# Performance work log

Measured on AMD Instinct MI355X. Metric: run time of the kernel, lower is better.

## Reference

```python
import jax, jax.numpy as jnp
import numpy as np

N_FEATURES = 256
SEQ_LEN = 128
N_HIDDEN = 30
N_LAYERS = 2
BATCH = 1024


def _lstm_layer(x, w_ih, w_hh, b_ih, b_hh):
    # x: [B, T, I]; w_ih: [4H, I]; w_hh: [4H, H]; biases: [4H]
    # PyTorch gate order: i, f, g, o
    B = x.shape[0]
    H = w_hh.shape[1]
    # precompute input contribution for all timesteps: [B, T, 4H]
    xg = jnp.einsum('bti,gi->btg', x, w_ih) + (b_ih + b_hh)
    xg = jnp.swapaxes(xg, 0, 1)  # [T, B, 4H]

    def step(carry, xg_t):
        h, c = carry
        gates = xg_t + h @ w_hh.T  # [B, 4H]
        i, f, g, o = jnp.split(gates, 4, axis=-1)
        i = jax.nn.sigmoid(i)
        f = jax.nn.sigmoid(f)
        g = jnp.tanh(g)
        o = jax.nn.sigmoid(o)
        c = f * c + i * g
        h = o * jnp.tanh(c)
        return (h, c), h

    h0 = jnp.zeros((B, H), dtype=x.dtype)
    c0 = jnp.zeros((B, H), dtype=x.dtype)
    _, hs = jax.lax.scan(step, (h0, c0), xg)
    return jnp.swapaxes(hs, 0, 1)  # [B, T, H]


def setup_inputs() -> dict:
    key = jax.random.key(0)
    ks = jax.random.split(key, 12)
    s_in = 1.0 / np.sqrt(N_HIDDEN)
    G = 4 * N_HIDDEN
    inp = {
        'x': jax.random.normal(ks[0], (BATCH, SEQ_LEN, N_FEATURES), dtype=jnp.float32),
        'w_ih0': jax.random.uniform(ks[1], (G, N_FEATURES), jnp.float32, -s_in, s_in),
        'w_hh0': jax.random.uniform(ks[2], (G, N_HIDDEN), jnp.float32, -s_in, s_in),
        'b_ih0': jax.random.uniform(ks[3], (G,), jnp.float32, -s_in, s_in),
        'b_hh0': jax.random.uniform(ks[4], (G,), jnp.float32, -s_in, s_in),
        'w_ih1': jax.random.uniform(ks[5], (G, N_HIDDEN), jnp.float32, -s_in, s_in),
        'w_hh1': jax.random.uniform(ks[6], (G, N_HIDDEN), jnp.float32, -s_in, s_in),
        'b_ih1': jax.random.uniform(ks[7], (G,), jnp.float32, -s_in, s_in),
        'b_hh1': jax.random.uniform(ks[8], (G,), jnp.float32, -s_in, s_in),
        'w_lin': jax.random.uniform(ks[9], (1, N_HIDDEN * SEQ_LEN), jnp.float32, -s_in, s_in),
        'b_lin': jax.random.uniform(ks[10], (1,), jnp.float32, -s_in, s_in),
    }
    return inp


def reference(x, w_ih0, w_hh0, b_ih0, b_hh0, w_ih1, w_hh1, b_ih1, b_hh1, w_lin, b_lin):
    h1 = _lstm_layer(x, w_ih0, w_hh0, b_ih0, b_hh0)   # [B, T, H]
    h2 = _lstm_layer(h1, w_ih1, w_hh1, b_ih1, b_hh1)  # [B, T, H]
    flat = h2.reshape(h2.shape[0], -1)                 # [B, T*H]
    return flat @ w_lin.T + b_lin                      # [B, 1]
```

## Files before the change

### kernel.cpp

```cpp
#include <hip/hip_runtime.h>

#define T_SEQ 128
#define NF 256
#define NH 30
#define NG 120
#define NBATCH 1024
#define M_ROWS (NBATCH * T_SEQ)

#define BIAS_OFF 0
#define BHI_OFF  1024
#define BLO_OFF  (BHI_OFF + 65536)
#define XG_OFF_B (BLO_OFF + 65536)

typedef __attribute__((ext_vector_type(8))) short short8;
typedef __attribute__((ext_vector_type(4))) float float4v;
typedef __attribute__((ext_vector_type(2))) float v2f;

__device__ __forceinline__ short bf16_of(float f) {
  union { float f; unsigned u; } v; v.f = f;
  unsigned r = v.u + 0x7fffu + ((v.u >> 16) & 1u);
  return (short)(r >> 16);
}
__device__ __forceinline__ float f_of_bf16(short s) {
  union { unsigned u; float f; } v; v.u = ((unsigned)(unsigned short)s) << 16;
  return v.f;
}

__device__ __forceinline__ float rl(float v, int j) {
  return __int_as_float(__builtin_amdgcn_readlane(__float_as_int(v), j));
}
__device__ __forceinline__ float fast_rcp(float x) { return __builtin_amdgcn_rcpf(x); }
__device__ __forceinline__ float act_mix(float x, float kIn, float kOut, float cOut) {
  float e = __expf(-kIn * x);
  float r = fast_rcp(1.0f + e);
  return fmaf(kOut, r, cOut);
}
__device__ __forceinline__ float tanh_fast(float x) {
  float e = __expf(-2.0f * x);
  float r = fast_rcp(1.0f + e);
  return fmaf(2.0f, r, -1.0f);
}
__device__ __forceinline__ v2f fma2(float s, v2f b, v2f c) {
  v2f a = {s, s};
  return __builtin_elementwise_fma(a, b, c);
}

__global__ void prep_kernel(const float* __restrict__ w_ih0,
                            const float* __restrict__ b_ih0,
                            const float* __restrict__ b_hh0,
                            unsigned char* __restrict__ ws) {
  int gid = blockIdx.x * 256 + threadIdx.x;
  float* bias = (float*)(ws + BIAS_OFF);
  if (gid < 128) bias[gid] = (gid < NG) ? (b_ih0[gid] + b_hh0[gid]) : 0.0f;

  int lane = gid & 63;
  int ts = gid >> 6;
  int t = ts >> 3, s = ts & 7;
  int n = s * 16 + (lane & 15);
  int k0 = t * 32 + (lane >> 4) * 8;

  short8 hi, lo;
#pragma unroll
  for (int j = 0; j < 8; ++j) {
    float v = (n < NG) ? w_ih0[n * NF + k0 + j] : 0.0f;
    short h = bf16_of(v);
    hi[j] = h;
    lo[j] = bf16_of(v - f_of_bf16(h));
  }
  *(short8*)(ws + BHI_OFF + (size_t)gid * 16) = hi;
  *(short8*)(ws + BLO_OFF + (size_t)gid * 16) = lo;
}

__global__ __launch_bounds__(256, 3) void gemm_xg(const float* __restrict__ x,
                                                  const unsigned char* __restrict__ ws,
                                                  float* __restrict__ xg) {
  __shared__ short lds_B[2][8 * 2 * 64 * 8];
  const int tid = threadIdx.x;
  const int lane = tid & 63;
  const int wave = tid >> 6;
  const int r15 = lane & 15;
  const int quad = lane >> 4;
  const int rowbase = blockIdx.x * 128 + wave * 32;

  const short* __restrict__ Bhi = (const short*)(ws + BHI_OFF);
  const short* __restrict__ Blo = (const short*)(ws + BLO_OFF);
  const float* __restrict__ bias = (const float*)(ws + BIAS_OFF);

  float4v acc[2][8];
#pragma unroll
  for (int s = 0; s < 8; ++s) {
    float b = bias[s * 16 + r15];
    float4v bv = {b, b, b, b};
    acc[0][s] = bv;
    acc[1][s] = bv;
  }

  const float* xptr[2];
  xptr[0] = x + (size_t)(rowbase + r15) * NF + quad * 8;
  xptr[1] = x + (size_t)(rowbase + 16 + r15) * NF + quad * 8;

#pragma unroll
  for (int i = 0; i < 2; ++i) {
    int s = wave * 2 + i;
    const short* ghi = Bhi + ((size_t)(0 * 8 + s) * 64 + lane) * 8;
    const short* glo = Blo + ((size_t)(0 * 8 + s) * 64 + lane) * 8;
    short* lhi = &lds_B[0][(s * 2 + 0) * 64 * 8];
    short* llo = &lds_B[0][(s * 2 + 1) * 64 * 8];
    __builtin_amdgcn_global_load_lds((const __attribute__((address_space(1))) void*)ghi,
                                     (__attribute__((address_space(3))) void*)lhi, 16, 0, 0);
    __builtin_amdgcn_global_load_lds((const __attribute__((address_space(1))) void*)glo,
                                     (__attribute__((address_space(3))) void*)llo, 16, 0, 0);
  }

  short8 ahi[2], alo[2];
#pragma unroll
  for (int g = 0; g < 2; ++g) {
    float4 p0 = *(const float4*)(xptr[g] + 0);
    float4 p1 = *(const float4*)(xptr[g] + 4);
    float f[8] = {p0.x, p0.y, p0.z, p0.w, p1.x, p1.y, p1.z, p1.w};
#pragma unroll
    for (int j = 0; j < 8; ++j) {
      short h = bf16_of(f[j]);
      ahi[g][j] = h;
      alo[g][j] = bf16_of(f[j] - f_of_bf16(h));
    }
  }
  __syncthreads();

  for (int t = 0; t < 8; ++t) {
    const int buf = t & 1;
    float4 anx[2][2];
    if (t < 7) {
#pragma unroll
      for (int i = 0; i < 2; ++i) {
        int s = wave * 2 + i;
        const short* ghi = Bhi + ((size_t)((t + 1) * 8 + s) * 64 + lane) * 8;
        const short* glo = Blo + ((size_t)((t + 1) * 8 + s) * 64 + lane) * 8;
        short* lhi = &lds_B[buf ^ 1][(s * 2 + 0) * 64 * 8];
        short* llo = &lds_B[buf ^ 1][(s * 2 + 1) * 64 * 8];
        __builtin_amdgcn_global_load_lds((const __attribute__((address_space(1))) void*)ghi,
                                         (__attribute__((address_space(3))) void*)lhi, 16, 0, 0);
        __builtin_amdgcn_global_load_lds((const __attribute__((address_space(1))) void*)glo,
                                         (__attribute__((address_space(3))) void*)llo, 16, 0, 0);
      }
#pragma unroll
      for (int g = 0; g < 2; ++g) {
        anx[g][0] = *(const float4*)(xptr[g] + (t + 1) * 32);
        anx[g][1] = *(const float4*)(xptr[g] + (t + 1) * 32 + 4);
      }
    }

#pragma unroll
    for (int s = 0; s < 8; ++s) {
      const short8 bh = *(const short8*)&lds_B[buf][((s * 2 + 0) * 64 + lane) * 8];
      const short8 bl = *(const short8*)&lds_B[buf][((s * 2 + 1) * 64 + lane) * 8];
#pragma unroll
      for (int g = 0; g < 2; ++g) {
        acc[g][s] = __builtin_amdgcn_mfma_f32_16x16x32_bf16(ahi[g], bh, acc[g][s], 0, 0, 0);
        acc[g][s] = __builtin_amdgcn_mfma_f32_16x16x32_bf16(ahi[g], bl, acc[g][s], 0, 0, 0);
        acc[g][s] = __builtin_amdgcn_mfma_f32_16x16x32_bf16(alo[g], bh, acc[g][s], 0, 0, 0);
      }
    }

    if (t < 7) {
#pragma unroll
      for (int g = 0; g < 2; ++g) {
        float f[8] = {anx[g][0].x, anx[g][0].y, anx[g][0].z, anx[g][0].w,
                      anx[g][1].x, anx[g][1].y, anx[g][1].z, anx[g][1].w};
#pragma unroll
        for (int j = 0; j < 8; ++j) {
          short h = bf16_of(f[j]);
          ahi[g][j] = h;
          alo[g][j] = bf16_of(f[j] - f_of_bf16(h));
        }
      }
    }
    __syncthreads();
  }

#pragma unroll
  for (int g = 0; g < 2; ++g) {
    const int row0 = rowbase + g * 16 + quad * 4;
#pragma unroll
    for (int s = 0; s < 8; ++s) {
      const int col = s * 16 + r15;
      if (col < NG) {
#pragma unroll
        for (int i = 0; i < 4; ++i) {
          xg[(size_t)(row0 + i) * NG + col] = acc[g][s][i];
        }
      }
    }
  }
}

__global__ __launch_bounds__(64, 1) void lstm_fused(const float* __restrict__ xg,
                                                    const float* __restrict__ w_hh0,
                                                    const float* __restrict__ w_ih1,
                                                    const float* __restrict__ w_hh1,
                                                    const float* __restrict__ b_ih1,
                                                    const float* __restrict__ b_hh1,
                                                    const float* __restrict__ w_lin,
                                                    const float* __restrict__ b_lin,
                                                    float* __restrict__ out) {
  const int b = blockIdx.x;
  const int lane = threadIdx.x;
  const bool hiHalf = lane >= 32;
  const int l = hiHalf ? (lane - 32) : lane;
  const int lc = (l < NH) ? l : (NH - 1);
  const int gA = hiHalf ? (60 + lc) : lc;
  const int gB = gA + NH;

  const float kInA = hiHalf ? 2.0f : 1.0f;
  const float kOutA = hiHalf ? 2.0f : 1.0f;
  const float cOutA = hiHalf ? -1.0f : 0.0f;

  v2f wAB0[NH], vAB1[NH], uAB1[NH];
#pragma unroll
  for (int j = 0; j < NH; ++j) {
    wAB0[j] = (v2f){w_hh0[gA * NH + j], w_hh0[gB * NH + j]};
    vAB1[j] = (v2f){w_ih1[gA * NH + j], w_ih1[gB * NH + j]};
    uAB1[j] = (v2f){w_hh1[gA * NH + j], w_hh1[gB * NH + j]};
  }
#pragma unroll
  for (int j = 0; j < NH; ++j) {
    asm volatile("" : "+v"(wAB0[j]), "+v"(vAB1[j]), "+v"(uAB1[j]));
  }
  const float bA1 = b_ih1[gA] + b_hh1[gA];
  const float bB1 = b_ih1[gB] + b_hh1[gB];

  const float* __restrict__ xgb = xg + (size_t)b * T_SEQ * NG;

  float a0A = act_mix(xgb[gA], kInA, kOutA, cOutA);
  float a0B = act_mix(xgb[gB], 1.0f, 1.0f, 0.0f);
  float gg0 = __shfl_down(a0A, 32);
  float oo0 = __shfl_down(a0B, 32);
  float c0 = a0A * gg0;
  float h0 = oo0 * tanh_fast(c0);
  float h1 = 0.0f, c1 = 0.0f, acc = 0.0f;
  float wl_cur = w_lin[lc];

#pragma unroll 1
  for (int t = 0; t < T_SEQ; ++t) {
    const int tn = (t + 1 < T_SEQ) ? (t + 1) : (T_SEQ - 1);
    float xnA = xgb[tn * NG + gA];
    float xnB = xgb[tn * NG + gB];
    float wl_nxt = w_lin[tn * NH + lc];

    v2f s1v = {bA1, bB1}, s1v2 = {0.0f, 0.0f};
    v2f s1u = {0.0f, 0.0f}, s1u2 = {0.0f, 0.0f};
    v2f s0n = {0.0f, 0.0f}, s0n2 = {0.0f, 0.0f};
#pragma unroll
    for (int j = 0; j < NH; j += 2) {
      float xj = rl(h0, j);
      float xj1 = rl(h0, j + 1);
      float hj = rl(h1, j);
      float hj1 = rl(h1, j + 1);
      s1v = fma2(xj, vAB1[j], s1v);
      s1u = fma2(hj, uAB1[j], s1u);
      s0n = fma2(xj, wAB0[j], s0n);
      s1v2 = fma2(xj1, vAB1[j + 1], s1v2);
      s1u2 = fma2(hj1, uAB1[j + 1], s1u2);
      s0n2 = fma2(xj1, wAB0[j + 1], s0n2);
    }
    v2f s1 = (s1v + s1v2) + (s1u + s1u2);
    v2f s0 = (s0n + s0n2) + (v2f){xnA, xnB};

    float a1A = act_mix(s1.x, kInA, kOutA, cOutA);
    float a1B = act_mix(s1.y, 1.0f, 1.0f, 0.0f);
    float gg1 = __shfl_down(a1A, 32);
    float oo1 = __shfl_down(a1B, 32);
    c1 = fmaf(a1B, c1, a1A * gg1);
    h1 = oo1 * tanh_fast(c1);
    acc = fmaf(h1, wl_cur, acc);

    a0A = act_mix(s0.x, kInA, kOutA, cOutA);
    a0B = act_mix(s0.y, 1.0f, 1.0f, 0.0f);
    gg0 = __shfl_down(a0A, 32);
    oo0 = __shfl_down(a0B, 32);
    c0 = fmaf(a0B, c0, a0A * gg0);
    h0 = oo0 * tanh_fast(c0);

    wl_cur = wl_nxt;
  }

  if (lane >= NH) acc = 0.0f;
#pragma unroll
  for (int off = 32; off > 0; off >>= 1) acc += __shfl_xor(acc, off);
  if (lane == 0) out[b] = acc + b_lin[0];
}

extern "C" void kernel_launch(void* const* d_in, const int* in_sizes, int n_in,
                              void* d_out, int out_size, void* d_ws, size_t ws_size,
                              hipStream_t stream) {
  (void)in_sizes; (void)n_in; (void)out_size; (void)ws_size;
  const float* x     = (const float*)d_in[0];
  const float* w_ih0 = (const float*)d_in[1];
  const float* w_hh0 = (const float*)d_in[2];
  const float* b_ih0 = (const float*)d_in[3];
  const float* b_hh0 = (const float*)d_in[4];
  const float* w_ih1 = (const float*)d_in[5];
  const float* w_hh1 = (const float*)d_in[6];
  const float* b_ih1 = (const float*)d_in[7];
  const float* b_hh1 = (const float*)d_in[8];
  const float* w_lin = (const float*)d_in[9];
  const float* b_lin = (const float*)d_in[10];
  unsigned char* ws = (unsigned char*)d_ws;
  float* out = (float*)d_out;
  float* xg = (float*)(ws + XG_OFF_B);

  prep_kernel<<<16, 256, 0, stream>>>(w_ih0, b_ih0, b_hh0, ws);
  gemm_xg<<<M_ROWS / 128, 256, 0, stream>>>(x, ws, xg);
  lstm_fused<<<NBATCH, 64, 0, stream>>>(xg, w_hh0, w_ih1, w_hh1,
                                        b_ih1, b_hh1, w_lin, b_lin, out);
}
```

Measured before the change: 312.0 us.

## Split fused LSTM into per-layer recurrences with MFMA GEMM for layer-1 input projection

Replaces the single fused two-layer recurrence kernel with a layer-0 recurrence kernel, a bf16 hi/lo split MFMA GEMM computing the layer-1 input projection for all timesteps, and a layer-1 recurrence kernel. Layer-0 hidden states are written in place into the xg buffer as packed bf16 hi/lo pairs. This cuts the per-step serial work in each recurrence from three 30-wide dot products to one, shortening the critical dependency chain. In exchange it adds two kernel launches, an extra round trip of the xg buffer through memory, and some precision loss from the split-bf16 layer-1 projection.

```diff
diff --git a/kernel.cpp b/kernel.cpp
--- a/kernel.cpp
+++ b/kernel.cpp
@@ -7,10 +7,13 @@
 #define NBATCH 1024
 #define M_ROWS (NBATCH * T_SEQ)
 
-#define BIAS_OFF 0
-#define BHI_OFF  1024
-#define BLO_OFF  (BHI_OFF + 65536)
-#define XG_OFF_B (BLO_OFF + 65536)
+#define BIAS0_OFF 0
+#define BIAS1_OFF 512
+#define B0HI_OFF  1024
+#define B0LO_OFF  (B0HI_OFF + 65536)
+#define B1HI_OFF  (B0LO_OFF + 65536)
+#define B1LO_OFF  (B1HI_OFF + 8192)
+#define XG_OFF_B  (B1LO_OFF + 8192)
 
 typedef __attribute__((ext_vector_type(8))) short short8;
 typedef __attribute__((ext_vector_type(4))) float float4v;
@@ -48,27 +51,50 @@
 __global__ void prep_kernel(const float* __restrict__ w_ih0,
                             const float* __restrict__ b_ih0,
                             const float* __restrict__ b_hh0,
+                            const float* __restrict__ w_ih1,
+                            const float* __restrict__ b_ih1,
+                            const float* __restrict__ b_hh1,
                             unsigned char* __restrict__ ws) {
   int gid = blockIdx.x * 256 + threadIdx.x;
-  float* bias = (float*)(ws + BIAS_OFF);
-  if (gid < 128) bias[gid] = (gid < NG) ? (b_ih0[gid] + b_hh0[gid]) : 0.0f;
-
-  int lane = gid & 63;
-  int ts = gid >> 6;
-  int t = ts >> 3, s = ts & 7;
-  int n = s * 16 + (lane & 15);
-  int k0 = t * 32 + (lane >> 4) * 8;
-
-  short8 hi, lo;
-#pragma unroll
-  for (int j = 0; j < 8; ++j) {
-    float v = (n < NG) ? w_ih0[n * NF + k0 + j] : 0.0f;
-    short h = bf16_of(v);
-    hi[j] = h;
-    lo[j] = bf16_of(v - f_of_bf16(h));
-  }
-  *(short8*)(ws + BHI_OFF + (size_t)gid * 16) = hi;
-  *(short8*)(ws + BLO_OFF + (size_t)gid * 16) = lo;
+  float* bias0 = (float*)(ws + BIAS0_OFF);
+  float* bias1 = (float*)(ws + BIAS1_OFF);
+  if (gid < 128) bias0[gid] = (gid < NG) ? (b_ih0[gid] + b_hh0[gid]) : 0.0f;
+
+  if (gid < 4096) {
+    int lane = gid & 63;
+    int ts = gid >> 6;
+    int t = ts >> 3, s = ts & 7;
+    int n = s * 16 + (lane & 15);
+    int k0 = t * 32 + (lane >> 4) * 8;
+    short8 hi, lo;
+#pragma unroll
+    for (int j = 0; j < 8; ++j) {
+      float v = (n < NG) ? w_ih0[n * NF + k0 + j] : 0.0f;
+      short h = bf16_of(v);
+      hi[j] = h;
+      lo[j] = bf16_of(v - f_of_bf16(h));
+    }
+    *(short8*)(ws + B0HI_OFF + (size_t)gid * 16) = hi;
+    *(short8*)(ws + B0LO_OFF + (size_t)gid * 16) = lo;
+  } else {
+    int q = gid - 4096;
+    if (q < 128) bias1[q] = (q < NG) ? (b_ih1[q] + b_hh1[q]) : 0.0f;
+    int lane = q & 63;
+    int s = q >> 6;
+    int n = s * 16 + (lane & 15);
+    int k0 = (lane >> 4) * 8;
+    short8 hi, lo;
+#pragma unroll
+    for (int j = 0; j < 8; ++j) {
+      int k = k0 + j;
+      float v = (n < NG && k < NH) ? w_ih1[n * NH + k] : 0.0f;
+      short h = bf16_of(v);
+      hi[j] = h;
+      lo[j] = bf16_of(v - f_of_bf16(h));
+    }
+    *(short8*)(ws + B1HI_OFF + (size_t)q * 16) = hi;
+    *(short8*)(ws + B1LO_OFF + (size_t)q * 16) = lo;
+  }
 }
 
 __global__ __launch_bounds__(256, 3) void gemm_xg(const float* __restrict__ x,
@@ -82,9 +108,9 @@
   const int quad = lane >> 4;
   const int rowbase = blockIdx.x * 128 + wave * 32;
 
-  const short* __restrict__ Bhi = (const short*)(ws + BHI_OFF);
-  const short* __restrict__ Blo = (const short*)(ws + BLO_OFF);
-  const float* __restrict__ bias = (const float*)(ws + BIAS_OFF);
+  const short* __restrict__ Bhi = (const short*)(ws + B0HI_OFF);
+  const short* __restrict__ Blo = (const short*)(ws + B0LO_OFF);
+  const float* __restrict__ bias = (const float*)(ws + BIAS0_OFF);
 
   float4v acc[2][8];
 #pragma unroll
@@ -194,15 +220,8 @@
   }
 }
 
-__global__ __launch_bounds__(64, 1) void lstm_fused(const float* __restrict__ xg,
-                                                    const float* __restrict__ w_hh0,
-                                                    const float* __restrict__ w_ih1,
-                                                    const float* __restrict__ w_hh1,
-                                                    const float* __restrict__ b_ih1,
-                                                    const float* __restrict__ b_hh1,
-                                                    const float* __restrict__ w_lin,
-                                                    const float* __restrict__ b_lin,
-                                                    float* __restrict__ out) {
+__global__ __attribute__((amdgpu_waves_per_eu(1, 1))) void __launch_bounds__(64)
+lstm0_kern(float* __restrict__ xg, const float* __restrict__ w_hh0) {
   const int b = blockIdx.x;
   const int lane = threadIdx.x;
   const bool hiHalf = lane >= 32;
@@ -215,73 +234,187 @@
   const float kOutA = hiHalf ? 2.0f : 1.0f;
   const float cOutA = hiHalf ? -1.0f : 0.0f;
 
-  v2f wAB0[NH], vAB1[NH], uAB1[NH];
+  v2f wAB0[NH];
 #pragma unroll
   for (int j = 0; j < NH; ++j) {
     wAB0[j] = (v2f){w_hh0[gA * NH + j], w_hh0[gB * NH + j]};
-    vAB1[j] = (v2f){w_ih1[gA * NH + j], w_ih1[gB * NH + j]};
-    uAB1[j] = (v2f){w_hh1[gA * NH + j], w_hh1[gB * NH + j]};
-  }
-#pragma unroll
-  for (int j = 0; j < NH; ++j) {
-    asm volatile("" : "+v"(wAB0[j]), "+v"(vAB1[j]), "+v"(uAB1[j]));
-  }
-  const float bA1 = b_ih1[gA] + b_hh1[gA];
-  const float bB1 = b_ih1[gB] + b_hh1[gB];
-
-  const float* __restrict__ xgb = xg + (size_t)b * T_SEQ * NG;
-
-  float a0A = act_mix(xgb[gA], kInA, kOutA, cOutA);
-  float a0B = act_mix(xgb[gB], 1.0f, 1.0f, 0.0f);
-  float gg0 = __shfl_down(a0A, 32);
-  float oo0 = __shfl_down(a0B, 32);
-  float c0 = a0A * gg0;
-  float h0 = oo0 * tanh_fast(c0);
-  float h1 = 0.0f, c1 = 0.0f, acc = 0.0f;
-  float wl_cur = w_lin[lc];
+  }
+
+  float* __restrict__ xgb = xg + (size_t)b * T_SEQ * NG;
+  float c0 = 0.0f, h0 = 0.0f;
+  float xA = xgb[gA], xB = xgb[gB];
 
 #pragma unroll 1
   for (int t = 0; t < T_SEQ; ++t) {
     const int tn = (t + 1 < T_SEQ) ? (t + 1) : (T_SEQ - 1);
-    float xnA = xgb[tn * NG + gA];
-    float xnB = xgb[tn * NG + gB];
-    float wl_nxt = w_lin[tn * NH + lc];
-
-    v2f s1v = {bA1, bB1}, s1v2 = {0.0f, 0.0f};
-    v2f s1u = {0.0f, 0.0f}, s1u2 = {0.0f, 0.0f};
-    v2f s0n = {0.0f, 0.0f}, s0n2 = {0.0f, 0.0f};
+    float xnA = xgb[(size_t)tn * NG + gA];
+    float xnB = xgb[(size_t)tn * NG + gB];
+
+    v2f s = {xA, xB}, s2 = {0.0f, 0.0f};
 #pragma unroll
     for (int j = 0; j < NH; j += 2) {
-      float xj = rl(h0, j);
-      float xj1 = rl(h0, j + 1);
+      float hj = rl(h0, j);
+      float hj1 = rl(h0, j + 1);
+      s = fma2(hj, wAB0[j], s);
+      s2 = fma2(hj1, wAB0[j + 1], s2);
+    }
+    s += s2;
+
+    float aA = act_mix(s.x, kInA, kOutA, cOutA);
+    float aB = act_mix(s.y, 1.0f, 1.0f, 0.0f);
+    float gg = __shfl_down(aA, 32);
+    float oo = __shfl_down(aB, 32);
+    c0 = fmaf(aB, c0, aA * gg);
+    h0 = oo * tanh_fast(c0);
+
+    short hh = bf16_of(h0);
+    unsigned hi = (unsigned short)hh;
+    unsigned lo = (unsigned short)bf16_of(h0 - f_of_bf16(hh));
+    unsigned pk = (hi << 16) | lo;
+    if (lane < 32) {
+      ((unsigned*)(xgb + (size_t)t * NG))[lane] = (lane < NH) ? pk : 0u;
+    }
+
+    xA = xnA;
+    xB = xnB;
+  }
+}
+
+__global__ __launch_bounds__(256) void gemm_xg1(float* __restrict__ xg,
+                                                const unsigned char* __restrict__ ws) {
+  __shared__ short lds_B[8 * 2 * 64 * 8];
+  const int tid = threadIdx.x;
+  const int lane = tid & 63;
+  const int wave = tid >> 6;
+  const int r15 = lane & 15;
+  const int quad = lane >> 4;
+  const int rowbase = blockIdx.x * 128 + wave * 32;
+
+  const short* __restrict__ Bhi = (const short*)(ws + B1HI_OFF);
+  const short* __restrict__ Blo = (const short*)(ws + B1LO_OFF);
+  const float* __restrict__ bias = (const float*)(ws + BIAS1_OFF);
+
+#pragma unroll
+  for (int i = 0; i < 2; ++i) {
+    int s = wave * 2 + i;
+    const short* ghi = Bhi + ((size_t)s * 64 + lane) * 8;
+    const short* glo = Blo + ((size_t)s * 64 + lane) * 8;
+    short* lhi = &lds_B[(s * 2 + 0) * 64 * 8];
+    short* llo = &lds_B[(s * 2 + 1) * 64 * 8];
+    __builtin_amdgcn_global_load_lds((const __attribute__((address_space(1))) void*)ghi,
+                                     (__attribute__((address_space(3))) void*)lhi, 16, 0, 0);
+    __builtin_amdgcn_global_load_lds((const __attribute__((address_space(1))) void*)glo,
+                                     (__attribute__((address_space(3))) void*)llo, 16, 0, 0);
+  }
+
+  float4v acc[2][8];
+#pragma unroll
+  for (int s = 0; s < 8; ++s) {
+    float b = bias[s * 16 + r15];
+    float4v bv = {b, b, b, b};
+    acc[0][s] = bv;
+    acc[1][s] = bv;
+  }
+
+  short8 ahi[2], alo[2];
+#pragma unroll
+  for (int g = 0; g < 2; ++g) {
+    const unsigned* ap =
+        (const unsigned*)(xg + (size_t)(rowbase + g * 16 + r15) * NG) + quad * 8;
+    uint4 q0 = *(const uint4*)(ap);
+    uint4 q1 = *(const uint4*)(ap + 4);
+    unsigned u[8] = {q0.x, q0.y, q0.z, q0.w, q1.x, q1.y, q1.z, q1.w};
+#pragma unroll
+    for (int j = 0; j < 8; ++j) {
+      ahi[g][j] = (short)(u[j] >> 16);
+      alo[g][j] = (short)(u[j] & 0xffffu);
+    }
+  }
+  __syncthreads();
+
+#pragma unroll
+  for (int s = 0; s < 8; ++s) {
+    const short8 bh = *(const short8*)&lds_B[((s * 2 + 0) * 64 + lane) * 8];
+    const short8 bl = *(const short8*)&lds_B[((s * 2 + 1) * 64 + lane) * 8];
+#pragma unroll
+    for (int g = 0; g < 2; ++g) {
+      acc[g][s] = __builtin_amdgcn_mfma_f32_16x16x32_bf16(ahi[g], bh, acc[g][s], 0, 0, 0);
+      acc[g][s] = __builtin_amdgcn_mfma_f32_16x16x32_bf16(ahi[g], bl, acc[g][s], 0, 0, 0);
+      acc[g][s] = __builtin_amdgcn_mfma_f32_16x16x32_bf16(alo[g], bh, acc[g][s], 0, 0, 0);
+    }
+  }
+
+#pragma unroll
+  for (int g = 0; g < 2; ++g) {
+    const int row0 = rowbase + g * 16 + quad * 4;
+#pragma unroll
+    for (int s = 0; s < 8; ++s) {
+      const int col = s * 16 + r15;
+      if (col < NG) {
+#pragma unroll
+        for (int i = 0; i < 4; ++i) {
+          xg[(size_t)(row0 + i) * NG + col] = acc[g][s][i];
+        }
+      }
+    }
+  }
+}
+
+__global__ __attribute__((amdgpu_waves_per_eu(1, 1))) void __launch_bounds__(64)
+lstm1_kern(const float* __restrict__ xg, const float* __restrict__ w_hh1,
+           const float* __restrict__ w_lin, const float* __restrict__ b_lin,
+           float* __restrict__ out) {
+  const int b = blockIdx.x;
+  const int lane = threadIdx.x;
+  const bool hiHalf = lane >= 32;
+  const int l = hiHalf ? (lane - 32) : lane;
+  const int lc = (l < NH) ? l : (NH - 1);
+  const int gA = hiHalf ? (60 + lc) : lc;
+  const int gB = gA + NH;
+
+  const float kInA = hiHalf ? 2.0f : 1.0f;
+  const float kOutA = hiHalf ? 2.0f : 1.0f;
+  const float cOutA = hiHalf ? -1.0f : 0.0f;
+
+  v2f uAB1[NH];
+#pragma unroll
+  for (int j = 0; j < NH; ++j) {
+    uAB1[j] = (v2f){w_hh1[gA * NH + j], w_hh1[gB * NH + j]};
+  }
+
+  const float* __restrict__ xgb = xg + (size_t)b * T_SEQ * NG;
+  float c1 = 0.0f, h1 = 0.0f, acc = 0.0f;
+  float xA = xgb[gA], xB = xgb[gB];
+  float wl = w_lin[lc];
+
+#pragma unroll 1
+  for (int t = 0; t < T_SEQ; ++t) {
+    const int tn = (t + 1 < T_SEQ) ? (t + 1) : (T_SEQ - 1);
+    float xnA = xgb[(size_t)tn * NG + gA];
+    float xnB = xgb[(size_t)tn * NG + gB];
+    float wln = w_lin[tn * NH + lc];
+
+    v2f s = {xA, xB}, s2 = {0.0f, 0.0f};
+#pragma unroll
+    for (int j = 0; j < NH; j += 2) {
       float hj = rl(h1, j);
       float hj1 = rl(h1, j + 1);
-      s1v = fma2(xj, vAB1[j], s1v);
-      s1u = fma2(hj, uAB1[j], s1u);
-      s0n = fma2(xj, wAB0[j], s0n);
-      s1v2 = fma2(xj1, vAB1[j + 1], s1v2);
-      s1u2 = fma2(hj1, uAB1[j + 1], s1u2);
-      s0n2 = fma2(xj1, wAB0[j + 1], s0n2);
-    }
-    v2f s1 = (s1v + s1v2) + (s1u + s1u2);
-    v2f s0 = (s0n + s0n2) + (v2f){xnA, xnB};
-
-    float a1A = act_mix(s1.x, kInA, kOutA, cOutA);
-    float a1B = act_mix(s1.y, 1.0f, 1.0f, 0.0f);
-    float gg1 = __shfl_down(a1A, 32);
-    float oo1 = __shfl_down(a1B, 32);
-    c1 = fmaf(a1B, c1, a1A * gg1);
-    h1 = oo1 * tanh_fast(c1);
-    acc = fmaf(h1, wl_cur, acc);
-
-    a0A = act_mix(s0.x, kInA, kOutA, cOutA);
-    a0B = act_mix(s0.y, 1.0f, 1.0f, 0.0f);
-    gg0 = __shfl_down(a0A, 32);
-    oo0 = __shfl_down(a0B, 32);
-    c0 = fmaf(a0B, c0, a0A * gg0);
-    h0 = oo0 * tanh_fast(c0);
-
-    wl_cur = wl_nxt;
+      s = fma2(hj, uAB1[j], s);
+      s2 = fma2(hj1, uAB1[j + 1], s2);
+    }
+    s += s2;
+
+    float aA = act_mix(s.x, kInA, kOutA, cOutA);
+    float aB = act_mix(s.y, 1.0f, 1.0f, 0.0f);
+    float gg = __shfl_down(aA, 32);
+    float oo = __shfl_down(aB, 32);
+    c1 = fmaf(aB, c1, aA * gg);
+    h1 = oo * tanh_fast(c1);
+    acc = fmaf(h1, wl, acc);
+
+    xA = xnA;
+    xB = xnB;
+    wl = wln;
   }
 
   if (lane >= NH) acc = 0.0f;
@@ -309,8 +442,9 @@
   float* out = (float*)d_out;
   float* xg = (float*)(ws + XG_OFF_B);
 
-  prep_kernel<<<16, 256, 0, stream>>>(w_ih0, b_ih0, b_hh0, ws);
+  prep_kernel<<<18, 256, 0, stream>>>(w_ih0, b_ih0, b_hh0, w_ih1, b_ih1, b_hh1, ws);
   gemm_xg<<<M_ROWS / 128, 256, 0, stream>>>(x, ws, xg);
-  lstm_fused<<<NBATCH, 64, 0, stream>>>(xg, w_hh0, w_ih1, w_hh1,
-                                        b_ih1, b_hh1, w_lin, b_lin, out);
-}
+  lstm0_kern<<<NBATCH, 64, 0, stream>>>(xg, w_hh0);
+  gemm_xg1<<<M_ROWS / 128, 256, 0, stream>>>(xg, ws);
+  lstm1_kern<<<NBATCH, 64, 0, stream>>>(xg, w_hh1, w_lin, b_lin, out);
+}
```

New measurement: 349.5 us. 12.0% more time.
